# Kernel tuning notes

Hardware: AMD Instinct MI355X
Metric: run time of the kernel (lower is better)

## Reference

```python
import jax, jax.numpy as jnp
import numpy as np

D_MODEL = 1024
NHEAD = 16
HEAD_DIM = D_MODEL // NHEAD
EPS = 1e-5


def layernorm(x, g, b):
    mu = jnp.mean(x, axis=-1, keepdims=True)
    var = jnp.mean(jnp.square(x - mu), axis=-1, keepdims=True)
    return (x - mu) * jax.lax.rsqrt(var + EPS) * g + b


def setup_inputs() -> dict:
    key = jax.random.key(0)
    ks = jax.random.split(key, 10)
    B, S, D = 8, 2048, D_MODEL
    s = 1.0 / np.sqrt(D)
    return {
        "x": jax.random.normal(ks[0], (B, S, D), dtype=jnp.float32),
        "wq": jax.random.normal(ks[1], (D, D), dtype=jnp.float32) * s,
        "wk": jax.random.normal(ks[2], (D, D), dtype=jnp.float32) * s,
        "wv": jax.random.normal(ks[3], (D, D), dtype=jnp.float32) * s,
        "ln1_g": jnp.ones((D,), dtype=jnp.float32),
        "ln1_b": jnp.zeros((D,), dtype=jnp.float32),
        "ln2_g": jnp.ones((D,), dtype=jnp.float32),
        "ln2_b": jnp.zeros((D,), dtype=jnp.float32),
        "w1": jax.random.normal(ks[4], (D, D), dtype=jnp.float32) * s,
        "b1": jnp.zeros((D,), dtype=jnp.float32),
        "w2": jax.random.normal(ks[5], (D, D), dtype=jnp.float32) * s,
        "b2": jnp.zeros((D,), dtype=jnp.float32),
    }


def reference(x, wq, wk, wv, ln1_g, ln1_b, ln2_g, ln2_b, w1, b1, w2, b2):
    B, S, D = x.shape
    H, Dh = NHEAD, HEAD_DIM
    xn = layernorm(x, ln1_g, ln1_b)
    # nn.Linear: y = x @ W.T (no bias for q/k/v)
    q = (xn @ wq.T).reshape(B, S, H, Dh)
    k = (xn @ wk.T).reshape(B, S, H, Dh)
    v = (xn @ wv.T).reshape(B, S, H, Dh)
    scale = 1.0 / jnp.sqrt(jnp.float32(Dh))
    scores = jnp.einsum("bqhd,bkhd->bhqk", q, k) * scale  # [B,H,S,S]
    attn = jax.nn.softmax(scores, axis=-1)
    att = jnp.einsum("bhqk,bkhd->bqhd", attn, v).reshape(B, S, D)
    xt = layernorm(xn + att, ln2_g, ln2_b)
    ffn = jax.nn.relu(xt @ w1.T + b1) @ w2.T + b2
    return xt + ffn
```

## Files before the change

### kernel.cpp

```cpp
#include <hip/hip_runtime.h>
#include <hip/hip_bf16.h>

typedef __bf16 bf16x8 __attribute__((ext_vector_type(8)));
typedef float f32x4 __attribute__((ext_vector_type(4)));
typedef float f32x16 __attribute__((ext_vector_type(16)));

#define MFMA_B16(a, b, c) __builtin_amdgcn_mfma_f32_16x16x32_bf16((a), (b), (c), 0, 0, 0)
#define MFMA32_B16(a, b, c) __builtin_amdgcn_mfma_f32_32x32x16_bf16((a), (b), (c), 0, 0, 0)
#define GLD16(g, l)                                                              \
    __builtin_amdgcn_global_load_lds((__attribute__((address_space(1))) void*)(g), \
                                     (__attribute__((address_space(3))) void*)(l), \
                                     16, 0, 0)

__device__ __forceinline__ float bfu2f(unsigned short u) {
    return __uint_as_float(((unsigned)u) << 16);
}
__device__ __forceinline__ unsigned short f2bfu(float f) {
    unsigned u = __float_as_uint(f);
    u += 0x7fffu + ((u >> 16) & 1u);
    return (unsigned short)(u >> 16);
}
__device__ __forceinline__ float fexp2(float x) {
#if __has_builtin(__builtin_amdgcn_exp2f)
    return __builtin_amdgcn_exp2f(x);
#else
    return __expf(x * 0.69314718f);
#endif
}
__device__ __forceinline__ unsigned cvtpk_bf16(float lo_, float hi_) {
    unsigned r;
    asm("v_cvt_pk_bf16_f32 %0, %1, %2" : "=v"(r) : "v"(lo_), "v"(hi_));
    return r;
}
__device__ __forceinline__ void plswap(unsigned& a, unsigned& b) {
#if __has_builtin(__builtin_amdgcn_permlane32_swap)
    typedef int v2i __attribute__((ext_vector_type(2)));
    v2i r = __builtin_amdgcn_permlane32_swap((int)a, (int)b, false, false);
    a = (unsigned)r.x;
    b = (unsigned)r.y;
#else
    unsigned pa_ = (unsigned)__shfl_xor((int)a, 32);
    unsigned pb_ = (unsigned)__shfl_xor((int)b, 32);
    bool hi = (threadIdx.x & 63) >= 32;
    unsigned na = hi ? pb_ : a;
    unsigned nb = hi ? b : pa_;
    a = na;
    b = nb;
#endif
}

__global__ __launch_bounds__(256) void cvt5_f32_bf16(const float* __restrict__ s0,
                                                     const float* __restrict__ s1,
                                                     const float* __restrict__ s2,
                                                     const float* __restrict__ s3,
                                                     const float* __restrict__ s4,
                                                     unsigned short* __restrict__ dst) {
    int wsel = blockIdx.x >> 10;
    int i = (blockIdx.x & 1023) * 256 + threadIdx.x;
    const float* src = s0;
    if (wsel == 1) src = s1;
    else if (wsel == 2) src = s2;
    else if (wsel == 3) src = s3;
    else if (wsel == 4) src = s4;
    float4 v = ((const float4*)src)[i];
    ((ushort4*)dst)[wsel * 262144 + i] =
        make_ushort4(f2bfu(v.x), f2bfu(v.y), f2bfu(v.z), f2bfu(v.w));
}

__global__ __launch_bounds__(256) void ln1_kernel(const float* __restrict__ in1,
                                                  const float* __restrict__ gam,
                                                  const float* __restrict__ bet,
                                                  unsigned short* __restrict__ outb) {
    int row = blockIdx.x, tid = threadIdx.x;
    size_t base = (size_t)row * 1024 + tid * 4;
    float4 v = *(const float4*)(in1 + base);
    float s = v.x + v.y + v.z + v.w;
    float sq = v.x * v.x + v.y * v.y + v.z * v.z + v.w * v.w;
#pragma unroll
    for (int m = 1; m < 64; m <<= 1) {
        s += __shfl_xor(s, m);
        sq += __shfl_xor(sq, m);
    }
    __shared__ float red[8];
    int w = tid >> 6;
    if ((tid & 63) == 0) { red[w] = s; red[w + 4] = sq; }
    __syncthreads();
    s = red[0] + red[1] + red[2] + red[3];
    sq = red[4] + red[5] + red[6] + red[7];
    float mean = s * (1.0f / 1024.0f);
    float var = fmaxf(sq * (1.0f / 1024.0f) - mean * mean, 0.0f);
    float rstd = rsqrtf(var + 1e-5f);
    float4 g4 = *(const float4*)(gam + tid * 4);
    float4 b4 = *(const float4*)(bet + tid * 4);
    *(ushort4*)(outb + base) = make_ushort4(
        f2bfu((v.x - mean) * rstd * g4.x + b4.x), f2bfu((v.y - mean) * rstd * g4.y + b4.y),
        f2bfu((v.z - mean) * rstd * g4.z + b4.z), f2bfu((v.w - mean) * rstd * g4.w + b4.w));
}

__global__ __launch_bounds__(256) void ln2_kernel(const unsigned short* __restrict__ in1,
                                                  const unsigned short* __restrict__ in2,
                                                  const float* __restrict__ gam,
                                                  const float* __restrict__ bet,
                                                  unsigned short* __restrict__ outb) {
    int row = blockIdx.x, tid = threadIdx.x;
    size_t base = (size_t)row * 1024 + tid * 4;
    ushort4 a = *(const ushort4*)(in1 + base);
    ushort4 c = *(const ushort4*)(in2 + base);
    float4 v = make_float4(bfu2f(a.x) + bfu2f(c.x), bfu2f(a.y) + bfu2f(c.y),
                           bfu2f(a.z) + bfu2f(c.z), bfu2f(a.w) + bfu2f(c.w));
    float s = v.x + v.y + v.z + v.w;
    float sq = v.x * v.x + v.y * v.y + v.z * v.z + v.w * v.w;
#pragma unroll
    for (int m = 1; m < 64; m <<= 1) {
        s += __shfl_xor(s, m);
        sq += __shfl_xor(sq, m);
    }
    __shared__ float red[8];
    int w = tid >> 6;
    if ((tid & 63) == 0) { red[w] = s; red[w + 4] = sq; }
    __syncthreads();
    s = red[0] + red[1] + red[2] + red[3];
    sq = red[4] + red[5] + red[6] + red[7];
    float mean = s * (1.0f / 1024.0f);
    float var = fmaxf(sq * (1.0f / 1024.0f) - mean * mean, 0.0f);
    float rstd = rsqrtf(var + 1e-5f);
    float4 g4 = *(const float4*)(gam + tid * 4);
    float4 b4 = *(const float4*)(bet + tid * 4);
    *(ushort4*)(outb + base) = make_ushort4(
        f2bfu((v.x - mean) * rstd * g4.x + b4.x), f2bfu((v.y - mean) * rstd * g4.y + b4.y),
        f2bfu((v.z - mean) * rstd * g4.z + b4.z), f2bfu((v.w - mean) * rstd * g4.w + b4.w));
}

template <bool OUTF32, bool BIAS, bool RELU, int RESID, bool VTOUT, bool QSC>
__global__ __launch_bounds__(256) void gemm_bt(const unsigned short* __restrict__ A,
                                               const unsigned short* __restrict__ Bw,
                                               const float* __restrict__ bias,
                                               const void* __restrict__ resid,
                                               void* __restrict__ Cout,
                                               int M, int N, int K) {
    __shared__ unsigned short As[128 * 32];
    __shared__ unsigned short Bs[128 * 32];
    int nt = N >> 7;
    int bid = blockIdx.x;
    int nwg = gridDim.x;
    int swz = (bid & 7) * (nwg >> 3) + (bid >> 3);
    int mt = swz / nt, ntl = swz % nt;
    int mbase = mt << 7, nbase = ntl << 7;
    int tid = threadIdx.x;
    int w = tid >> 6, l = tid & 63;
    int wr = w >> 1, wc = w & 1;
    int lg = l >> 4, lr = l & 15;

    const unsigned short* a0 = A + (size_t)(mbase + (tid >> 2)) * K + (tid & 3) * 8;
    const unsigned short* a1 = A + (size_t)(mbase + 64 + (tid >> 2)) * K + (tid & 3) * 8;
    const unsigned short* b0 = Bw + (size_t)(nbase + (tid >> 2)) * K + (tid & 3) * 8;
    const unsigned short* b1 = Bw + (size_t)(nbase + 64 + (tid >> 2)) * K + (tid & 3) * 8;
    unsigned short* As_d0 = As + w * 512;
    unsigned short* As_d1 = As + 2048 + w * 512;
    unsigned short* Bs_d0 = Bs + w * 512;
    unsigned short* Bs_d1 = Bs + 2048 + w * 512;

    const unsigned short* Af = As + (wr * 64 + lr) * 32 + lg * 8;
    const unsigned short* Bf = Bs + (wc * 64 + lr) * 32 + lg * 8;

    f32x4 acc[4][4] = {};

    for (int kb = 0; kb < K; kb += 32) {
        __syncthreads();
        GLD16(a0, As_d0);
        GLD16(a1, As_d1);
        GLD16(b0, Bs_d0);
        GLD16(b1, Bs_d1);
        a0 += 32; a1 += 32; b0 += 32; b1 += 32;
        __syncthreads();
        bf16x8 af[4], bf[4];
#pragma unroll
        for (int m = 0; m < 4; m++) af[m] = *(const bf16x8*)(Af + m * 16 * 32);
#pragma unroll
        for (int n = 0; n < 4; n++) bf[n] = *(const bf16x8*)(Bf + n * 16 * 32);
        __builtin_amdgcn_s_setprio(1);
#pragma unroll
        for (int m = 0; m < 4; m++)
#pragma unroll
            for (int n = 0; n < 4; n++)
                acc[m][n] = MFMA_B16(af[m], bf[n], acc[m][n]);
        __builtin_amdgcn_s_setprio(0);
    }

#pragma unroll
    for (int m = 0; m < 4; m++) {
        int row = mbase + wr * 64 + m * 16 + lg * 4;
#pragma unroll
        for (int n = 0; n < 4; n++) {
            int col = nbase + wc * 64 + n * 16 + lr;
            float bv = BIAS ? bias[col] : 0.0f;
            if constexpr (VTOUT) {
                int bb = row >> 11, ss = row & 2047;
                int hh = col >> 6, dd = col & 63;
                unsigned short t4[4];
#pragma unroll
                for (int j = 0; j < 4; j++) t4[j] = f2bfu(acc[m][n][j]);
                size_t vtidx = ((size_t)((bb * 16 + hh) * 64 + dd)) * 2048 + ss;
                *(uint2*)((unsigned short*)Cout + vtidx) = *(uint2*)t4;
            } else {
#pragma unroll
                for (int j = 0; j < 4; j++) {
                    float v = acc[m][n][j] + bv;
                    if (QSC) v *= 0.18033688f;
                    if (RELU) v = fmaxf(v, 0.0f);
                    size_t idx = (size_t)(row + j) * N + col;
                    if (RESID == 2) v += bfu2f(((const unsigned short*)resid)[idx]);
                    if (OUTF32) ((float*)Cout)[idx] = v;
                    else ((unsigned short*)Cout)[idx] = f2bfu(v);
                }
            }
        }
    }
}

__global__ __launch_bounds__(512) void attn_kernel(const unsigned short* __restrict__ qq,
                                                   const unsigned short* __restrict__ kk,
                                                   const unsigned short* __restrict__ vT,
                                                   unsigned short* __restrict__ attb) {
    __shared__ unsigned short Ks[2][64 * 64];
    __shared__ unsigned short Vs[2][64 * 64];

    int bid = blockIdx.x;
    int swz = (bid & 7) * (gridDim.x >> 3) + (bid >> 3);
    int qi = swz & 7, h = (swz >> 3) & 15, b = swz >> 7;
    int tid = threadIdx.x, w = tid >> 6, l = tid & 63;
    int lo = l & 31, hi = l >> 5;
    int q0 = qi * 256 + w * 32;

    const unsigned short* qp = qq + ((size_t)((b * 2048 + q0 + lo) * 16 + h)) * 64 + hi * 8;
    bf16x8 qf[4];
#pragma unroll
    for (int kc = 0; kc < 4; kc++) qf[kc] = *(const bf16x8*)(qp + kc * 16);

    int srow = w * 8 + (l >> 3);
    int schunk = (l & 7) ^ ((l >> 3) & 7);
    const unsigned short* ksrc = kk + ((size_t)((b * 2048 + srow) * 16 + h)) * 64 + schunk * 8;
    const unsigned short* vsrc = vT + ((size_t)((b * 16 + h) * 64 + srow)) * 2048 + schunk * 8;

    f32x16 od0 = {}, od1 = {};
    float ssum = 0.f;

    GLD16(ksrc, &Ks[0][w * 512]);
    GLD16(vsrc, &Vs[0][w * 512]);
    ksrc += 65536;
    vsrc += 64;
    asm volatile("s_waitcnt vmcnt(0)");
    __syncthreads();

    int cur = 0;
    for (int t = 0; t < 32; t++) {
        if (t < 31) {
            GLD16(ksrc, &Ks[cur ^ 1][w * 512]);
            GLD16(vsrc, &Vs[cur ^ 1][w * 512]);
            ksrc += 65536;
            vsrc += 64;
        }
        const unsigned short* Kb = &Ks[cur][0];
        f32x16 sacc[2];
        __builtin_amdgcn_s_setprio(1);
#pragma unroll
        for (int tt = 0; tt < 2; tt++) {
            f32x16 s = {};
            int row = tt * 32 + lo;
#pragma unroll
            for (int kc = 0; kc < 4; kc++) {
                bf16x8 a = *(const bf16x8*)(Kb + row * 64 + (((kc * 2 + hi) ^ (row & 7)) << 3));
                s = MFMA32_B16(a, qf[kc], s);
            }
            sacc[tt] = s;
        }
        __builtin_amdgcn_s_setprio(0);
        float p[32];
        float psum = 0.f;
#pragma unroll
        for (int tt = 0; tt < 2; tt++)
#pragma unroll
            for (int r = 0; r < 16; r++) {
                float e = fexp2(sacc[tt][r] - 16.0f);
                p[tt * 16 + r] = e;
                psum += e;
            }
        psum += __shfl_xor(psum, 32);
        ssum += psum;
        const unsigned short* Vb = &Vs[cur][0];
#pragma unroll
        for (int tt = 0; tt < 2; tt++) {
            unsigned wv[8];
#pragma unroll
            for (int i = 0; i < 8; i++) wv[i] = cvtpk_bf16(p[tt * 16 + 2 * i], p[tt * 16 + 2 * i + 1]);
            plswap(wv[0], wv[2]);
            plswap(wv[1], wv[3]);
            plswap(wv[4], wv[6]);
            plswap(wv[5], wv[7]);
            union { unsigned u[4]; bf16x8 v; } c0, c1;
            c0.u[0] = wv[0]; c0.u[1] = wv[1]; c0.u[2] = wv[2]; c0.u[3] = wv[3];
            c1.u[0] = wv[4]; c1.u[1] = wv[5]; c1.u[2] = wv[6]; c1.u[3] = wv[7];
            __builtin_amdgcn_s_setprio(1);
#pragma unroll
            for (int sub = 0; sub < 2; sub++) {
                int ks = tt * 2 + sub;
                bf16x8 pa = sub ? c1.v : c0.v;
                int slot = ((ks * 2 + hi) ^ (lo & 7)) << 3;
                bf16x8 v0 = *(const bf16x8*)(Vb + lo * 64 + slot);
                bf16x8 v1 = *(const bf16x8*)(Vb + (32 + lo) * 64 + slot);
                od0 = MFMA32_B16(pa, v0, od0);
                od1 = MFMA32_B16(pa, v1, od1);
            }
            __builtin_amdgcn_s_setprio(0);
        }
        asm volatile("s_waitcnt vmcnt(0)");
        __syncthreads();
        cur ^= 1;
    }

#pragma unroll
    for (int r = 0; r < 16; r++) {
        int crow = (r & 3) + ((r >> 2) << 3) + (hi << 2);
        float rs = 1.0f / __shfl(ssum, crow);
        int q = q0 + crow;
        size_t base = ((size_t)((b * 2048 + q) * 16 + h)) * 64;
        attb[base + lo] = f2bfu(od0[r] * rs);
        attb[base + 32 + lo] = f2bfu(od1[r] * rs);
    }
}

extern "C" void kernel_launch(void* const* d_in, const int* in_sizes, int n_in,
                              void* d_out, int out_size, void* d_ws, size_t ws_size,
                              hipStream_t stream) {
    const float* x = (const float*)d_in[0];
    const float* wq = (const float*)d_in[1];
    const float* wk = (const float*)d_in[2];
    const float* wv = (const float*)d_in[3];
    const float* ln1_g = (const float*)d_in[4];
    const float* ln1_b = (const float*)d_in[5];
    const float* ln2_g = (const float*)d_in[6];
    const float* ln2_b = (const float*)d_in[7];
    const float* w1 = (const float*)d_in[8];
    const float* b1 = (const float*)d_in[9];
    const float* w2 = (const float*)d_in[10];
    const float* b2 = (const float*)d_in[11];

    const size_t NB = 33554432;
    char* ws = (char*)d_ws;
    unsigned short* xn_b = (unsigned short*)(ws);
    unsigned short* q_b = (unsigned short*)(ws + NB);
    unsigned short* k_b = (unsigned short*)(ws + 2 * NB);
    unsigned short* vT_b = (unsigned short*)(ws + 3 * NB);
    unsigned short* att_b = (unsigned short*)(ws + 4 * NB);
    unsigned short* wq_b = (unsigned short*)(ws + 5 * NB);
    unsigned short* wk_b = wq_b + 1048576;
    unsigned short* wv_b = wk_b + 1048576;
    unsigned short* w1_b = wv_b + 1048576;
    unsigned short* w2_b = w1_b + 1048576;
    unsigned short* xt_b = q_b;
    unsigned short* h_b = k_b;

    dim3 blk(256);
    cvt5_f32_bf16<<<5120, blk, 0, stream>>>(wq, wk, wv, w1, w2, wq_b);
    ln1_kernel<<<16384, blk, 0, stream>>>(x, ln1_g, ln1_b, xn_b);

    gemm_bt<false, false, false, 0, false, true><<<1024, blk, 0, stream>>>(
        xn_b, wq_b, nullptr, nullptr, q_b, 16384, 1024, 1024);
    gemm_bt<false, false, false, 0, false, false><<<1024, blk, 0, stream>>>(
        xn_b, wk_b, nullptr, nullptr, k_b, 16384, 1024, 1024);
    gemm_bt<false, false, false, 0, true, false><<<1024, blk, 0, stream>>>(
        xn_b, wv_b, nullptr, nullptr, vT_b, 16384, 1024, 1024);

    attn_kernel<<<1024, dim3(512), 0, stream>>>(q_b, k_b, vT_b, att_b);

    ln2_kernel<<<16384, blk, 0, stream>>>(xn_b, att_b, ln2_g, ln2_b, xt_b);

    gemm_bt<false, true, true, 0, false, false><<<1024, blk, 0, stream>>>(
        xt_b, w1_b, b1, nullptr, h_b, 16384, 1024, 1024);
    gemm_bt<true, true, false, 2, false, false><<<1024, blk, 0, stream>>>(
        h_b, w2_b, b2, xt_b, d_out, 16384, 1024, 1024);
}
```

Baseline: 467.8 us.

## Fuse QKV GEMMs, retile GEMM to 256x128 with triple-buffered LDS, MFMA row sums

Replaces the 128x128 single-buffered GEMM with a 256x128 tile, 512-thread kernel using BK=64, a three-stage global-to-LDS pipeline and XOR-swizzled LDS layout. The three Q/K/V projections are fused into one N=3072 GEMM over contiguous bf16 weights, with per-column routing of outputs. In attention, the softmax row sum is computed by an extra MFMA against a ones vector instead of scalar adds and a shuffle. This aims to raise MFMA utilization and cut launch and load-wait overhead, at the cost of much more LDS per block (144KB), which limits occupancy.

Measured after the change: 477.5 us. +2.1%, slower.

```diff
diff --git a/kernel.cpp b/kernel.cpp
--- a/kernel.cpp
+++ b/kernel.cpp
@@ -131,87 +131,120 @@
         f2bfu((v.z - mean) * rstd * g4.z + b4.z), f2bfu((v.w - mean) * rstd * g4.w + b4.w));
 }
 
-template <bool OUTF32, bool BIAS, bool RELU, int RESID, bool VTOUT, bool QSC>
-__global__ __launch_bounds__(256) void gemm_bt(const unsigned short* __restrict__ A,
-                                               const unsigned short* __restrict__ Bw,
-                                               const float* __restrict__ bias,
-                                               const void* __restrict__ resid,
-                                               void* __restrict__ Cout,
-                                               int M, int N, int K) {
-    __shared__ unsigned short As[128 * 32];
-    __shared__ unsigned short Bs[128 * 32];
+template <int MODE>
+__global__ __launch_bounds__(512, 2) void gemm3(const unsigned short* __restrict__ A,
+                                                const unsigned short* __restrict__ Bw,
+                                                const float* __restrict__ bias,
+                                                const unsigned short* __restrict__ resid,
+                                                void* __restrict__ O0,
+                                                void* __restrict__ O1,
+                                                void* __restrict__ O2,
+                                                int M, int N, int K) {
+    __shared__ unsigned short As[3][256 * 64];
+    __shared__ unsigned short Bs[3][128 * 64];
     int nt = N >> 7;
     int bid = blockIdx.x;
     int nwg = gridDim.x;
     int swz = (bid & 7) * (nwg >> 3) + (bid >> 3);
     int mt = swz / nt, ntl = swz % nt;
-    int mbase = mt << 7, nbase = ntl << 7;
+    int mbase = mt << 8, nbase = ntl << 7;
     int tid = threadIdx.x;
     int w = tid >> 6, l = tid & 63;
-    int wr = w >> 1, wc = w & 1;
-    int lg = l >> 4, lr = l & 15;
-
-    const unsigned short* a0 = A + (size_t)(mbase + (tid >> 2)) * K + (tid & 3) * 8;
-    const unsigned short* a1 = A + (size_t)(mbase + 64 + (tid >> 2)) * K + (tid & 3) * 8;
-    const unsigned short* b0 = Bw + (size_t)(nbase + (tid >> 2)) * K + (tid & 3) * 8;
-    const unsigned short* b1 = Bw + (size_t)(nbase + 64 + (tid >> 2)) * K + (tid & 3) * 8;
-    unsigned short* As_d0 = As + w * 512;
-    unsigned short* As_d1 = As + 2048 + w * 512;
-    unsigned short* Bs_d0 = Bs + w * 512;
-    unsigned short* Bs_d1 = Bs + 2048 + w * 512;
-
-    const unsigned short* Af = As + (wr * 64 + lr) * 32 + lg * 8;
-    const unsigned short* Bf = Bs + (wc * 64 + lr) * 32 + lg * 8;
-
-    f32x4 acc[4][4] = {};
-
-    for (int kb = 0; kb < K; kb += 32) {
-        __syncthreads();
-        GLD16(a0, As_d0);
-        GLD16(a1, As_d1);
-        GLD16(b0, Bs_d0);
-        GLD16(b1, Bs_d1);
-        a0 += 32; a1 += 32; b0 += 32; b1 += 32;
-        __syncthreads();
-        bf16x8 af[4], bf[4];
-#pragma unroll
-        for (int m = 0; m < 4; m++) af[m] = *(const bf16x8*)(Af + m * 16 * 32);
-#pragma unroll
-        for (int n = 0; n < 4; n++) bf[n] = *(const bf16x8*)(Bf + n * 16 * 32);
-        __builtin_amdgcn_s_setprio(1);
-#pragma unroll
-        for (int m = 0; m < 4; m++)
-#pragma unroll
-            for (int n = 0; n < 4; n++)
-                acc[m][n] = MFMA_B16(af[m], bf[n], acc[m][n]);
-        __builtin_amdgcn_s_setprio(0);
-    }
-
-#pragma unroll
-    for (int m = 0; m < 4; m++) {
-        int row = mbase + wr * 64 + m * 16 + lg * 4;
-#pragma unroll
-        for (int n = 0; n < 4; n++) {
-            int col = nbase + wc * 64 + n * 16 + lr;
-            float bv = BIAS ? bias[col] : 0.0f;
-            if constexpr (VTOUT) {
-                int bb = row >> 11, ss = row & 2047;
-                int hh = col >> 6, dd = col & 63;
-                unsigned short t4[4];
-#pragma unroll
-                for (int j = 0; j < 4; j++) t4[j] = f2bfu(acc[m][n][j]);
-                size_t vtidx = ((size_t)((bb * 16 + hh) * 64 + dd)) * 2048 + ss;
-                *(uint2*)((unsigned short*)Cout + vtidx) = *(uint2*)t4;
+    int wm = w >> 2, wn = w & 3;
+    int lr = l & 15, lg = l >> 4;
+
+    int srow = tid >> 3;
+    int csrc = (tid & 7) ^ (srow & 7);
+    const unsigned short* ag = A + (size_t)(mbase + srow) * K + csrc * 8;
+    const unsigned short* bg = Bw + (size_t)(nbase + srow) * K + csrc * 8;
+
+    auto stage = [&](int t) {
+        int buf = t % 3;
+        const unsigned short* a = ag + (size_t)t * 64;
+        const unsigned short* b = bg + (size_t)t * 64;
+#pragma unroll
+        for (int j = 0; j < 4; j++)
+            GLD16(a + (size_t)j * 64 * K, &As[buf][j * 4096 + w * 512]);
+#pragma unroll
+        for (int j = 0; j < 2; j++)
+            GLD16(b + (size_t)j * 64 * K, &Bs[buf][j * 4096 + w * 512]);
+    };
+
+    f32x4 acc[8][2] = {};
+    int NT = K >> 6;
+
+    stage(0);
+    stage(1);
+    asm volatile("s_waitcnt vmcnt(6)" ::: "memory");
+    __builtin_amdgcn_s_barrier();
+
+    for (int t = 0; t < NT; t++) {
+        int buf = t % 3;
+        if (t + 2 < NT) stage(t + 2);
+        const unsigned short* Ab = &As[buf][(wm * 128) * 64];
+        const unsigned short* Bb = &Bs[buf][(wn * 32) * 64];
+        bf16x8 af[8][2], bf[2][2];
+#pragma unroll
+        for (int m = 0; m < 8; m++)
+#pragma unroll
+            for (int ks = 0; ks < 2; ks++)
+                af[m][ks] = *(const bf16x8*)(Ab + (m * 16 + lr) * 64 +
+                                             (((ks * 4 + lg) ^ (lr & 7)) << 3));
+#pragma unroll
+        for (int n = 0; n < 2; n++)
+#pragma unroll
+            for (int ks = 0; ks < 2; ks++)
+                bf[n][ks] = *(const bf16x8*)(Bb + (n * 16 + lr) * 64 +
+                                             (((ks * 4 + lg) ^ (lr & 7)) << 3));
+#pragma unroll
+        for (int m = 0; m < 8; m++)
+#pragma unroll
+            for (int n = 0; n < 2; n++)
+#pragma unroll
+                for (int ks = 0; ks < 2; ks++)
+                    acc[m][n] = MFMA_B16(af[m][ks], bf[n][ks], acc[m][n]);
+        if (t < NT - 1) {
+            if (t + 2 < NT) asm volatile("s_waitcnt vmcnt(6)" ::: "memory");
+            else asm volatile("s_waitcnt vmcnt(0)" ::: "memory");
+            __builtin_amdgcn_s_barrier();
+        }
+    }
+
+#pragma unroll
+    for (int m = 0; m < 8; m++) {
+        int row = mbase + wm * 128 + m * 16 + lg * 4;
+#pragma unroll
+        for (int n = 0; n < 2; n++) {
+            int col = nbase + wn * 32 + n * 16 + lr;
+            if constexpr (MODE == 0) {
+                int wsel = col >> 10;
+                int cl = col & 1023;
+                if (wsel == 2) {
+                    int hh = cl >> 6, dd = cl & 63;
+                    int bb = row >> 11, ss = row & 2047;
+                    unsigned short t4[4];
+#pragma unroll
+                    for (int j = 0; j < 4; j++) t4[j] = f2bfu(acc[m][n][j]);
+                    size_t vtidx = ((size_t)((bb * 16 + hh) * 64 + dd)) * 2048 + ss;
+                    *(uint2*)((unsigned short*)O2 + vtidx) = *(uint2*)t4;
+                } else {
+                    unsigned short* out = (wsel == 0) ? (unsigned short*)O0 : (unsigned short*)O1;
+                    float sc = (wsel == 0) ? 0.18033688f : 1.0f;
+#pragma unroll
+                    for (int j = 0; j < 4; j++)
+                        out[(size_t)(row + j) * 1024 + cl] = f2bfu(acc[m][n][j] * sc);
+                }
             } else {
+                float bv = bias[col];
 #pragma unroll
                 for (int j = 0; j < 4; j++) {
                     float v = acc[m][n][j] + bv;
-                    if (QSC) v *= 0.18033688f;
-                    if (RELU) v = fmaxf(v, 0.0f);
                     size_t idx = (size_t)(row + j) * N + col;
-                    if (RESID == 2) v += bfu2f(((const unsigned short*)resid)[idx]);
-                    if (OUTF32) ((float*)Cout)[idx] = v;
-                    else ((unsigned short*)Cout)[idx] = f2bfu(v);
+                    if constexpr (MODE == 1) {
+                        ((unsigned short*)O0)[idx] = f2bfu(fmaxf(v, 0.0f));
+                    } else {
+                        ((float*)O0)[idx] = v + bfu2f(resid[idx]);
+                    }
                 }
             }
         }
@@ -237,13 +270,17 @@
 #pragma unroll
     for (int kc = 0; kc < 4; kc++) qf[kc] = *(const bf16x8*)(qp + kc * 16);
 
+    union { unsigned short us[8]; bf16x8 v; } ones_u;
+#pragma unroll
+    for (int i = 0; i < 8; i++) ones_u.us[i] = 0x3F80;
+    bf16x8 onesf = ones_u.v;
+
     int srow = w * 8 + (l >> 3);
     int schunk = (l & 7) ^ ((l >> 3) & 7);
     const unsigned short* ksrc = kk + ((size_t)((b * 2048 + srow) * 16 + h)) * 64 + schunk * 8;
     const unsigned short* vsrc = vT + ((size_t)((b * 16 + h) * 64 + srow)) * 2048 + schunk * 8;
 
-    f32x16 od0 = {}, od1 = {};
-    float ssum = 0.f;
+    f32x16 od0 = {}, od1 = {}, ssm = {};
 
     GLD16(ksrc, &Ks[0][w * 512]);
     GLD16(vsrc, &Vs[0][w * 512]);
@@ -276,17 +313,11 @@
         }
         __builtin_amdgcn_s_setprio(0);
         float p[32];
-        float psum = 0.f;
 #pragma unroll
         for (int tt = 0; tt < 2; tt++)
 #pragma unroll
-            for (int r = 0; r < 16; r++) {
-                float e = fexp2(sacc[tt][r] - 16.0f);
-                p[tt * 16 + r] = e;
-                psum += e;
-            }
-        psum += __shfl_xor(psum, 32);
-        ssum += psum;
+            for (int r = 0; r < 16; r++)
+                p[tt * 16 + r] = fexp2(sacc[tt][r] - 16.0f);
         const unsigned short* Vb = &Vs[cur][0];
 #pragma unroll
         for (int tt = 0; tt < 2; tt++) {
@@ -310,6 +341,7 @@
                 bf16x8 v1 = *(const bf16x8*)(Vb + (32 + lo) * 64 + slot);
                 od0 = MFMA32_B16(pa, v0, od0);
                 od1 = MFMA32_B16(pa, v1, od1);
+                ssm = MFMA32_B16(pa, onesf, ssm);
             }
             __builtin_amdgcn_s_setprio(0);
         }
@@ -321,7 +353,7 @@
 #pragma unroll
     for (int r = 0; r < 16; r++) {
         int crow = (r & 3) + ((r >> 2) << 3) + (hi << 2);
-        float rs = 1.0f / __shfl(ssum, crow);
+        float rs = 1.0f / ssm[r];
         int q = q0 + crow;
         size_t base = ((size_t)((b * 2048 + q) * 16 + h)) * 64;
         attb[base + lo] = f2bfu(od0[r] * rs);
@@ -353,9 +385,7 @@
     unsigned short* vT_b = (unsigned short*)(ws + 3 * NB);
     unsigned short* att_b = (unsigned short*)(ws + 4 * NB);
     unsigned short* wq_b = (unsigned short*)(ws + 5 * NB);
-    unsigned short* wk_b = wq_b + 1048576;
-    unsigned short* wv_b = wk_b + 1048576;
-    unsigned short* w1_b = wv_b + 1048576;
+    unsigned short* w1_b = wq_b + 3145728;
     unsigned short* w2_b = w1_b + 1048576;
     unsigned short* xt_b = q_b;
     unsigned short* h_b = k_b;
@@ -364,19 +394,15 @@
     cvt5_f32_bf16<<<5120, blk, 0, stream>>>(wq, wk, wv, w1, w2, wq_b);
     ln1_kernel<<<16384, blk, 0, stream>>>(x, ln1_g, ln1_b, xn_b);
 
-    gemm_bt<false, false, false, 0, false, true><<<1024, blk, 0, stream>>>(
-        xn_b, wq_b, nullptr, nullptr, q_b, 16384, 1024, 1024);
-    gemm_bt<false, false, false, 0, false, false><<<1024, blk, 0, stream>>>(
-        xn_b, wk_b, nullptr, nullptr, k_b, 16384, 1024, 1024);
-    gemm_bt<false, false, false, 0, true, false><<<1024, blk, 0, stream>>>(
-        xn_b, wv_b, nullptr, nullptr, vT_b, 16384, 1024, 1024);
+    gemm3<0><<<1536, dim3(512), 0, stream>>>(xn_b, wq_b, nullptr, nullptr,
+                                             q_b, k_b, vT_b, 16384, 3072, 1024);
 
     attn_kernel<<<1024, dim3(512), 0, stream>>>(q_b, k_b, vT_b, att_b);
 
     ln2_kernel<<<16384, blk, 0, stream>>>(xn_b, att_b, ln2_g, ln2_b, xt_b);
 
-    gemm_bt<false, true, true, 0, false, false><<<1024, blk, 0, stream>>>(
-        xt_b, w1_b, b1, nullptr, h_b, 16384, 1024, 1024);
-    gemm_bt<true, true, false, 2, false, false><<<1024, blk, 0, stream>>>(
-        h_b, w2_b, b2, xt_b, d_out, 16384, 1024, 1024);
-}
+    gemm3<1><<<512, dim3(512), 0, stream>>>(xt_b, w1_b, b1, nullptr,
+                                            h_b, nullptr, nullptr, 16384, 1024, 1024);
+    gemm3<2><<<512, dim3(512), 0, stream>>>(h_b, w2_b, b2, xt_b,
+                                            d_out, nullptr, nullptr, 16384, 1024, 1024);
+}
```
